# Performance work log

Hardware: AMD Instinct MI355X
Metric: run time of the kernel (lower is better)

The kernel has to match this reference:

```python
import jax, jax.numpy as jnp
import numpy as np

H, W = 16, 64
HK, WK = 7, 11
NUM_HEADS = 8
DIM = 512
HEAD_DIM = DIM // NUM_HEADS
SCALE = HEAD_DIM ** -0.5
N = H * W


def _local_mask():
    # Additive mask [N, N]: 0 inside the local window, -inf outside.
    # Equivalent to the torch loop: token (h,w) attends to (i,j) with
    # |i-h| <= HK//2 and |j-w| <= WK//2 (odd kernel, centered crop).
    h = jnp.arange(H)
    w = jnp.arange(W)
    hh, ww = jnp.meshgrid(h, w, indexing='ij')  # [H, W]
    q_h = hh.reshape(-1)  # [N]
    q_w = ww.reshape(-1)
    in_win = (jnp.abs(q_h[:, None] - q_h[None, :]) <= HK // 2) & \
             (jnp.abs(q_w[:, None] - q_w[None, :]) <= WK // 2)
    return jnp.where(in_win, 0.0, -jnp.inf).astype(jnp.float32)  # [N, N]


def setup_inputs() -> dict:
    key = jax.random.key(0)
    k1, k2, k3 = jax.random.split(key, 3)
    x = jax.random.normal(k1, (64, N, DIM), dtype=jnp.float32)
    w_qkv = jax.random.normal(k2, (DIM, 3 * DIM), dtype=jnp.float32) * 0.02
    w_proj = jax.random.normal(k3, (DIM, DIM), dtype=jnp.float32) * 0.02
    b_proj = jnp.zeros((DIM,), dtype=jnp.float32)
    return {"x": x, "w_qkv": w_qkv, "w_proj": w_proj, "b_proj": b_proj}


def reference(x, w_qkv, w_proj, b_proj):
    B = x.shape[0]
    mask = _local_mask()  # [N, N]
    qkv = (x @ w_qkv).reshape(B, N, 3, NUM_HEADS, HEAD_DIM)
    q = qkv[:, :, 0].transpose(0, 2, 1, 3) * SCALE  # [B, h, N, d]
    k = qkv[:, :, 1].transpose(0, 2, 1, 3)
    v = qkv[:, :, 2].transpose(0, 2, 1, 3)
    attn = jnp.einsum('bhnd,bhmd->bhnm', q, k) + mask  # [B, h, N, N]
    attn = jax.nn.softmax(attn, axis=-1)
    out = jnp.einsum('bhnm,bhmd->bhnd', attn, v)
    out = out.transpose(0, 2, 1, 3).reshape(B, N, DIM)
    return out @ w_proj + b_proj
```

## Files before the change

### kernel.cpp

```cpp
#include <hip/hip_runtime.h>
#include <hip/hip_bf16.h>
#include <stdint.h>

#define HGRID   16
#define WGRID   64
#define NTOK    1024
#define BATCH   64
#define NHEADS  8
#define HDIM    64
#define DMODEL  512
#define BH_TOT  512
#define QK_SCALE (0.125f * 1.44269504089f)

typedef __attribute__((ext_vector_type(8))) short short8;
typedef __attribute__((ext_vector_type(4))) float floatx4;

__device__ __forceinline__ short f2bf(float f) {
    union { float f; uint32_t u; } c{f};
    uint32_t r = (c.u + 0x7fffu + ((c.u >> 16) & 1u)) >> 16;
    return (short)r;
}

__device__ __forceinline__ void gload_lds16(const void* g, void* l) {
    auto gp = (const __attribute__((address_space(1))) void*)(uintptr_t)g;
    auto lp = (__attribute__((address_space(3))) void*)(uint32_t)(uintptr_t)l;
    __builtin_amdgcn_global_load_lds(gp, lp, 16, 0, 0);
}

__global__ __launch_bounds__(256)
void cast_x_kernel(const float* __restrict__ in, short* __restrict__ out) {
    size_t i = (size_t)blockIdx.x * 256 + threadIdx.x;
    const float4* in4 = (const float4*)in;
    float4 a = in4[i * 2];
    float4 b = in4[i * 2 + 1];
    short8 o;
    o[0] = f2bf(a.x); o[1] = f2bf(a.y); o[2] = f2bf(a.z); o[3] = f2bf(a.w);
    o[4] = f2bf(b.x); o[5] = f2bf(b.y); o[6] = f2bf(b.z); o[7] = f2bf(b.w);
    *(short8*)(out + i * 8) = o;
}

__global__ __launch_bounds__(256)
void tcast_kernel(const float* __restrict__ in, short* __restrict__ out, int R, int C) {
    __shared__ short tile[64][72];
    int r0 = blockIdx.x * 64, c0 = blockIdx.y * 64;
    int t = threadIdx.x;
#pragma unroll
    for (int i = 0; i < 16; i++) {
        int s = i * 256 + t;
        int r = s >> 6, c = s & 63;
        tile[r][c] = f2bf(in[(size_t)(r0 + r) * C + c0 + c]);
    }
    __syncthreads();
#pragma unroll
    for (int i = 0; i < 16; i++) {
        int s = i * 256 + t;
        int c = s >> 6, r = s & 63;
        out[(size_t)(c0 + c) * R + r0 + r] = tile[r][c];
    }
}

template <int MODE>
__global__ __launch_bounds__(256)
void gemm_kernel(const short* __restrict__ A, const short* __restrict__ Bm,
                 short* __restrict__ qo, short* __restrict__ ko, short* __restrict__ vo,
                 float* __restrict__ outf, const float* __restrict__ bias) {
    __shared__ short As[128 * 32];
    __shared__ short Bs[128 * 32];
    const int bn = blockIdx.x, bm = blockIdx.y;
    const int t = threadIdx.x;
    const int w = t >> 6;
    const int l = t & 63;
    const int wm = w >> 1, wn = w & 1;
    const int lq = l & 15, quad = l >> 4;

    const floatx4 zero = {0.f, 0.f, 0.f, 0.f};
    floatx4 acc[4][4];
#pragma unroll
    for (int i = 0; i < 4; i++)
#pragma unroll
        for (int j = 0; j < 4; j++) acc[i][j] = zero;

    const short* Ab = A + (size_t)bm * 128 * 512;
    const short* Bb = Bm + (size_t)bn * 128 * 512;

    for (int k0 = 0; k0 < 512; k0 += 32) {
        __syncthreads();
#pragma unroll
        for (int i = 0; i < 2; i++) {
            int s = i * 256 + t;
            int r = s >> 2, c8 = (s & 3) * 8;
            gload_lds16(Ab + (size_t)r * 512 + k0 + c8, &As[s * 8]);
            gload_lds16(Bb + (size_t)r * 512 + k0 + c8, &Bs[s * 8]);
        }
        __syncthreads();

        short8 af[4], bfr[4];
#pragma unroll
        for (int mi = 0; mi < 4; mi++)
            af[mi] = *(const short8*)&As[(wm * 64 + mi * 16 + lq) * 32 + quad * 8];
#pragma unroll
        for (int ni = 0; ni < 4; ni++)
            bfr[ni] = *(const short8*)&Bs[(wn * 64 + ni * 16 + lq) * 32 + quad * 8];
#pragma unroll
        for (int mi = 0; mi < 4; mi++)
#pragma unroll
            for (int ni = 0; ni < 4; ni++)
                acc[mi][ni] = __builtin_amdgcn_mfma_f32_16x16x32_bf16(
                    af[mi], bfr[ni], acc[mi][ni], 0, 0, 0);
    }

#pragma unroll
    for (int mi = 0; mi < 4; mi++)
#pragma unroll
        for (int ni = 0; ni < 4; ni++)
#pragma unroll
            for (int r = 0; r < 4; r++) {
                int row = bm * 128 + wm * 64 + mi * 16 + quad * 4 + r;
                int col = bn * 128 + wn * 64 + ni * 16 + lq;
                float val = acc[mi][ni][r];
                if (MODE == 0) {
                    int bidx = row >> 10, tok = row & 1023;
                    int which = col >> 9, hd = (col >> 6) & 7, dd = col & 63;
                    size_t didx = (((size_t)bidx * NHEADS + hd) * NTOK + tok) * HDIM + dd;
                    if (which == 0)       qo[didx] = f2bf(val * QK_SCALE);
                    else if (which == 1)  ko[didx] = f2bf(val);
                    else                  vo[didx] = f2bf(val);
                } else {
                    outf[(size_t)row * DMODEL + col] = val + bias[col];
                }
            }
}

__global__ __launch_bounds__(256)
void tv_kernel(const short* __restrict__ v, short* __restrict__ vT) {
    __shared__ short tile[64][72];
    int tt = blockIdx.x;
    int bh = blockIdx.y;
    int t = threadIdx.x;
    const short* src = v + ((size_t)bh * NTOK + tt * 64) * HDIM;
#pragma unroll
    for (int i = 0; i < 2; i++) {
        int s = i * 256 + t;
        int r = s >> 3, c8 = (s & 7) * 8;
        *(short8*)&tile[r][c8] = *(const short8*)(src + r * HDIM + c8);
    }
    __syncthreads();
    short* dst = vT + (size_t)bh * HDIM * NTOK + tt * 64;
#pragma unroll
    for (int i = 0; i < 2; i++) {
        int s = i * 256 + t;
        int d = s & 63, t0 = (s >> 6) * 8;
        short8 g;
#pragma unroll
        for (int j = 0; j < 8; j++) g[j] = tile[t0 + j][d];
        *(short8*)(dst + (size_t)d * NTOK + t0) = g;
    }
}

__global__ __launch_bounds__(256)
void attn_kernel(const short* __restrict__ q, const short* __restrict__ k,
                 const short* __restrict__ vT, short* __restrict__ ao) {
    const int bid = blockIdx.x;
    const int h = (bid >> 3) & 15;
    const int bh = (bid & 7) + 8 * (bid >> 7);
    const int b = bh >> 3, head = bh & 7;
    const int t = threadIdx.x;
    const int w = t >> 6;
    const int l = t & 63;
    const int lq = l & 15, quad = l >> 4;

    __shared__ short Kc[64][72];
    __shared__ short Vc[80][72];
    __shared__ short Pc[4][16][40];

    const int s_w = (w == 0) ? 0 : (w == 1) ? 8 : (w == 2) ? 24 : 32;

    const short* qbp = q + ((size_t)bh * NTOK + h * 64 + w * 16 + lq) * HDIM + quad * 8;
    short8 qa0 = *(const short8*)(qbp);
    short8 qa1 = *(const short8*)(qbp + 32);

    bool ok[2][4];
#pragma unroll
    for (int nt = 0; nt < 2; nt++)
#pragma unroll
        for (int r = 0; r < 4; r++) {
            int kw_g = s_w + nt * 16 + lq;
            int qi = w * 16 + quad * 4 + r;
            int dw = kw_g - qi;
            ok[nt][r] = (dw <= 5) && (dw >= -5);
        }

    const floatx4 zero = {0.f, 0.f, 0.f, 0.f};
    floatx4 O[5];
#pragma unroll
    for (int i = 0; i < 5; i++) O[i] = zero;

    if (t < 64) Vc[64][t] = (short)0x3F80;

    const int kh0 = (h - 3 < 0) ? 0 : h - 3;
    const int kh1 = (h + 3 > HGRID - 1) ? HGRID - 1 : h + 3;

    for (int kh = kh0; kh <= kh1; ++kh) {
        __syncthreads();
        {
            const short* kb = k + ((size_t)bh * NTOK + kh * 64) * HDIM;
            const short* vb = vT + (size_t)bh * HDIM * NTOK + kh * 64;
#pragma unroll
            for (int i = 0; i < 2; i++) {
                int s = i * 256 + t;
                int r = s >> 3, c8 = (s & 7) * 8;
                *(short8*)&Kc[r][c8] = *(const short8*)(kb + r * HDIM + c8);
                *(short8*)&Vc[r][c8] = *(const short8*)(vb + (size_t)r * NTOK + c8);
            }
        }
        __syncthreads();

        floatx4 S[2];
#pragma unroll
        for (int nt = 0; nt < 2; nt++) {
            S[nt] = zero;
            short8 b0 = *(const short8*)&Kc[s_w + nt * 16 + lq][quad * 8];
            short8 b1 = *(const short8*)&Kc[s_w + nt * 16 + lq][quad * 8 + 32];
            S[nt] = __builtin_amdgcn_mfma_f32_16x16x32_bf16(qa0, b0, S[nt], 0, 0, 0);
            S[nt] = __builtin_amdgcn_mfma_f32_16x16x32_bf16(qa1, b1, S[nt], 0, 0, 0);
        }

#pragma unroll
        for (int nt = 0; nt < 2; nt++)
#pragma unroll
            for (int r = 0; r < 4; r++) {
                float p = ok[nt][r] ? exp2f(S[nt][r]) : 0.f;
                Pc[w][quad * 4 + r][nt * 16 + lq] = f2bf(p);
            }

        short8 pa = *(const short8*)&Pc[w][lq][quad * 8];
#pragma unroll
        for (int dt = 0; dt < 5; dt++) {
            short8 vf = *(const short8*)&Vc[dt * 16 + lq][s_w + quad * 8];
            O[dt] = __builtin_amdgcn_mfma_f32_16x16x32_bf16(pa, vf, O[dt], 0, 0, 0);
        }
    }

    float inv[4];
#pragma unroll
    for (int r = 0; r < 4; r++) {
        float s = __shfl(O[4][r], l & 48);
        inv[r] = 1.0f / s;
    }

#pragma unroll
    for (int dt = 0; dt < 4; dt++)
#pragma unroll
        for (int r = 0; r < 4; r++) {
            int qi = w * 16 + quad * 4 + r;
            int d = dt * 16 + lq;
            float o = O[dt][r] * inv[r];
            ao[((size_t)b * NTOK + h * 64 + qi) * DMODEL + head * HDIM + d] = f2bf(o);
        }
}

extern "C" void kernel_launch(void* const* d_in, const int* in_sizes, int n_in,
                              void* d_out, int out_size, void* d_ws, size_t ws_size,
                              hipStream_t stream) {
    const float* x      = (const float*)d_in[0];
    const float* w_qkv  = (const float*)d_in[1];
    const float* w_proj = (const float*)d_in[2];
    const float* b_proj = (const float*)d_in[3];
    float* out = (float*)d_out;

    const size_t SZ_X    = (size_t)BATCH * NTOK * DMODEL * 2;
    const size_t SZ_HEAD = (size_t)BH_TOT * NTOK * HDIM * 2;
    char* p = (char*)d_ws;
    short* xb     = (short*)p; p += SZ_X;
    short* wqkvT  = (short*)p; p += (size_t)1536 * 512 * 2;
    short* wprojT = (short*)p; p += (size_t)512 * 512 * 2;
    short* qb     = (short*)p; p += SZ_HEAD;
    short* kb     = (short*)p; p += SZ_HEAD;
    short* vb     = (short*)p; p += SZ_HEAD;
    short* vTb    = (short*)p; p += SZ_HEAD;
    short* ao     = xb;

    cast_x_kernel<<<dim3((BATCH * NTOK * DMODEL) / (256 * 8)), dim3(256), 0, stream>>>(x, xb);
    tcast_kernel<<<dim3(512 / 64, 1536 / 64), dim3(256), 0, stream>>>(w_qkv, wqkvT, 512, 1536);
    tcast_kernel<<<dim3(512 / 64, 512 / 64), dim3(256), 0, stream>>>(w_proj, wprojT, 512, 512);
    gemm_kernel<0><<<dim3(1536 / 128, 65536 / 128), dim3(256), 0, stream>>>(
        xb, wqkvT, qb, kb, vb, nullptr, nullptr);
    tv_kernel<<<dim3(NTOK / 64, BH_TOT), dim3(256), 0, stream>>>(vb, vTb);
    attn_kernel<<<dim3(HGRID * BH_TOT), dim3(256), 0, stream>>>(qb, kb, vTb, ao);
    gemm_kernel<1><<<dim3(512 / 128, 65536 / 128), dim3(256), 0, stream>>>(
        ao, wprojT, nullptr, nullptr, nullptr, out, b_proj);
}
```

Before: 559.6 us.

## Rewrite GEMM with triple-buffered LDS pipeline and fuse V transpose into epilogue

```diff
diff --git a/kernel.cpp b/kernel.cpp
--- a/kernel.cpp
+++ b/kernel.cpp
@@ -60,18 +60,33 @@
 }
 
 template <int MODE>
-__global__ __launch_bounds__(256)
+__global__ __launch_bounds__(512, 4)
 void gemm_kernel(const short* __restrict__ A, const short* __restrict__ Bm,
-                 short* __restrict__ qo, short* __restrict__ ko, short* __restrict__ vo,
+                 short* __restrict__ qo, short* __restrict__ ko, short* __restrict__ vTo,
                  float* __restrict__ outf, const float* __restrict__ bias) {
-    __shared__ short As[128 * 32];
-    __shared__ short Bs[128 * 32];
-    const int bn = blockIdx.x, bm = blockIdx.y;
+    constexpr int NBN = (MODE == 0) ? 6 : 2;
+    constexpr int NWG = (MODE == 0) ? 3072 : 1024;
+    __shared__ char lds[73728];
+    char* ldsc = (char*)lds;
+
+    int bid = blockIdx.x;
+    bid = (bid & 7) * (NWG >> 3) + (bid >> 3);
+    const int bn = bid % NBN, bm = bid / NBN;
+
     const int t = threadIdx.x;
-    const int w = t >> 6;
-    const int l = t & 63;
-    const int wm = w >> 1, wn = w & 1;
+    const int w = t >> 6, l = t & 63;
     const int lq = l & 15, quad = l >> 4;
+    const int wm = w >> 2, wn = w & 3;
+
+    const int sw = ((quad ^ ((lq >> 1) & 3)) << 4);
+    const int a_off = (wm * 64 + lq) * 64 + sw;
+    const int b_off = 8192 + (wn * 64 + lq) * 64 + sw;
+
+    const int srow = t >> 2;
+    const int scol = ((t & 3) ^ ((t >> 3) & 3)) * 8;
+    const short* sA = A + (size_t)bm * 128 * 512 + (size_t)srow * 512 + scol;
+    const short* sB = Bm + (size_t)bn * 256 * 512 + (size_t)srow * 512 + scol;
+    const int t16 = t * 16;
 
     const floatx4 zero = {0.f, 0.f, 0.f, 0.f};
     floatx4 acc[4][4];
@@ -80,80 +95,108 @@
 #pragma unroll
         for (int j = 0; j < 4; j++) acc[i][j] = zero;
 
-    const short* Ab = A + (size_t)bm * 128 * 512;
-    const short* Bb = Bm + (size_t)bn * 128 * 512;
-
-    for (int k0 = 0; k0 < 512; k0 += 32) {
-        __syncthreads();
-#pragma unroll
-        for (int i = 0; i < 2; i++) {
-            int s = i * 256 + t;
-            int r = s >> 2, c8 = (s & 3) * 8;
-            gload_lds16(Ab + (size_t)r * 512 + k0 + c8, &As[s * 8]);
-            gload_lds16(Bb + (size_t)r * 512 + k0 + c8, &Bs[s * 8]);
-        }
-        __syncthreads();
-
+#define STAGE(T, BUFI) do {                                            \
+        char* _b = ldsc + (BUFI) * 24576;                              \
+        gload_lds16(sA + (T) * 32, _b + t16);                          \
+        gload_lds16(sB + (T) * 32, _b + 8192 + t16);                   \
+        gload_lds16(sB + 128 * 512 + (T) * 32, _b + 16384 + t16);      \
+    } while (0)
+
+    STAGE(0, 0);
+    STAGE(1, 1);
+    asm volatile("s_waitcnt vmcnt(3)" ::: "memory");
+    __builtin_amdgcn_s_barrier();
+
+#pragma unroll
+    for (int T = 0; T < 16; ++T) {
+        const int cur = T % 3;
+        if (T + 2 < 16) STAGE(T + 2, (T + 2) % 3);
+
+        const char* base = ldsc + cur * 24576;
         short8 af[4], bfr[4];
 #pragma unroll
         for (int mi = 0; mi < 4; mi++)
-            af[mi] = *(const short8*)&As[(wm * 64 + mi * 16 + lq) * 32 + quad * 8];
+            af[mi] = *(const short8*)(base + a_off + mi * 1024);
 #pragma unroll
         for (int ni = 0; ni < 4; ni++)
-            bfr[ni] = *(const short8*)&Bs[(wn * 64 + ni * 16 + lq) * 32 + quad * 8];
+            bfr[ni] = *(const short8*)(base + b_off + ni * 1024);
+        asm volatile("s_waitcnt lgkmcnt(0)" ::: "memory");
+        __builtin_amdgcn_sched_barrier(0);
+        __builtin_amdgcn_s_setprio(1);
 #pragma unroll
         for (int mi = 0; mi < 4; mi++)
 #pragma unroll
             for (int ni = 0; ni < 4; ni++)
                 acc[mi][ni] = __builtin_amdgcn_mfma_f32_16x16x32_bf16(
                     af[mi], bfr[ni], acc[mi][ni], 0, 0, 0);
-    }
-
-#pragma unroll
-    for (int mi = 0; mi < 4; mi++)
-#pragma unroll
-        for (int ni = 0; ni < 4; ni++)
-#pragma unroll
-            for (int r = 0; r < 4; r++) {
-                int row = bm * 128 + wm * 64 + mi * 16 + quad * 4 + r;
-                int col = bn * 128 + wn * 64 + ni * 16 + lq;
-                float val = acc[mi][ni][r];
-                if (MODE == 0) {
-                    int bidx = row >> 10, tok = row & 1023;
-                    int which = col >> 9, hd = (col >> 6) & 7, dd = col & 63;
-                    size_t didx = (((size_t)bidx * NHEADS + hd) * NTOK + tok) * HDIM + dd;
-                    if (which == 0)       qo[didx] = f2bf(val * QK_SCALE);
-                    else if (which == 1)  ko[didx] = f2bf(val);
-                    else                  vo[didx] = f2bf(val);
-                } else {
-                    outf[(size_t)row * DMODEL + col] = val + bias[col];
+        __builtin_amdgcn_s_setprio(0);
+        __builtin_amdgcn_sched_barrier(0);
+        if (T < 14) asm volatile("s_waitcnt vmcnt(3)" ::: "memory");
+        else        asm volatile("s_waitcnt vmcnt(0)" ::: "memory");
+        __builtin_amdgcn_s_barrier();
+    }
+#undef STAGE
+
+    if (MODE == 1) {
+#pragma unroll
+        for (int ni = 0; ni < 4; ni++) {
+            int col = bn * 256 + wn * 64 + ni * 16 + lq;
+            float bv = bias[col];
+#pragma unroll
+            for (int mi = 0; mi < 4; mi++)
+#pragma unroll
+                for (int r = 0; r < 4; r++) {
+                    int row = bm * 128 + wm * 64 + mi * 16 + quad * 4 + r;
+                    outf[(size_t)row * DMODEL + col] = acc[mi][ni][r] + bv;
+                }
+        }
+        return;
+    }
+
+    const int which = bn >> 1;
+    if (which < 2) {
+        short* dst = which ? ko : qo;
+        const float sc = which ? 1.0f : QK_SCALE;
+        const int hd = (bn & 1) * 4 + wn;
+#pragma unroll
+        for (int mi = 0; mi < 4; mi++)
+#pragma unroll
+            for (int ni = 0; ni < 4; ni++)
+#pragma unroll
+                for (int r = 0; r < 4; r++) {
+                    int row = bm * 128 + wm * 64 + mi * 16 + quad * 4 + r;
+                    int tok = row & 1023, bidx = row >> 10;
+                    dst[(((size_t)bidx * NHEADS + hd) * NTOK + tok) * HDIM + ni * 16 + lq] =
+                        f2bf(acc[mi][ni][r] * sc);
+                }
+    } else {
+        short* Tb = (short*)ldsc;
+        __syncthreads();
+#pragma unroll
+        for (int mi = 0; mi < 4; mi++)
+#pragma unroll
+            for (int ni = 0; ni < 4; ni++) {
+                int cl = wn * 64 + ni * 16 + lq;
+#pragma unroll
+                for (int rp = 0; rp < 2; rp++) {
+                    int rw = wm * 64 + mi * 16 + quad * 4 + rp * 2;
+                    uint32_t lo = (uint32_t)(uint16_t)f2bf(acc[mi][ni][rp * 2]);
+                    uint32_t hi = (uint32_t)(uint16_t)f2bf(acc[mi][ni][rp * 2 + 1]);
+                    *(uint32_t*)&Tb[cl * 140 + rw] = lo | (hi << 16);
                 }
             }
-}
-
-__global__ __launch_bounds__(256)
-void tv_kernel(const short* __restrict__ v, short* __restrict__ vT) {
-    __shared__ short tile[64][72];
-    int tt = blockIdx.x;
-    int bh = blockIdx.y;
-    int t = threadIdx.x;
-    const short* src = v + ((size_t)bh * NTOK + tt * 64) * HDIM;
-#pragma unroll
-    for (int i = 0; i < 2; i++) {
-        int s = i * 256 + t;
-        int r = s >> 3, c8 = (s & 7) * 8;
-        *(short8*)&tile[r][c8] = *(const short8*)(src + r * HDIM + c8);
-    }
-    __syncthreads();
-    short* dst = vT + (size_t)bh * HDIM * NTOK + tt * 64;
-#pragma unroll
-    for (int i = 0; i < 2; i++) {
-        int s = i * 256 + t;
-        int d = s & 63, t0 = (s >> 6) * 8;
-        short8 g;
-#pragma unroll
-        for (int j = 0; j < 8; j++) g[j] = tile[t0 + j][d];
-        *(short8*)(dst + (size_t)d * NTOK + t0) = g;
+        __syncthreads();
+        int cl = t >> 1, part = t & 1;
+        int hd = (bn & 1) * 4 + (cl >> 6), dd = cl & 63;
+        int bidx = bm >> 3, tokb = (bm & 7) * 128 + part * 64;
+        short* dst = vTo + (((size_t)bidx * NHEADS + hd) * HDIM + dd) * NTOK + tokb;
+#pragma unroll
+        for (int j = 0; j < 8; j++) {
+            uint2 x = *(const uint2*)&Tb[cl * 140 + part * 64 + j * 8];
+            uint2 y = *(const uint2*)&Tb[cl * 140 + part * 64 + j * 8 + 4];
+            uint4 o; o.x = x.x; o.y = x.y; o.z = y.x; o.w = y.y;
+            *(uint4*)(dst + j * 8) = o;
+        }
     }
 }
 
@@ -276,17 +319,13 @@
     short* wprojT = (short*)p; p += (size_t)512 * 512 * 2;
     short* qb     = (short*)p; p += SZ_HEAD;
     short* kb     = (short*)p; p += SZ_HEAD;
-    short* vb     = (short*)p; p += SZ_HEAD;
     short* vTb    = (short*)p; p += SZ_HEAD;
     short* ao     = xb;
 
     cast_x_kernel<<<dim3((BATCH * NTOK * DMODEL) / (256 * 8)), dim3(256), 0, stream>>>(x, xb);
     tcast_kernel<<<dim3(512 / 64, 1536 / 64), dim3(256), 0, stream>>>(w_qkv, wqkvT, 512, 1536);
     tcast_kernel<<<dim3(512 / 64, 512 / 64), dim3(256), 0, stream>>>(w_proj, wprojT, 512, 512);
-    gemm_kernel<0><<<dim3(1536 / 128, 65536 / 128), dim3(256), 0, stream>>>(
-        xb, wqkvT, qb, kb, vb, nullptr, nullptr);
-    tv_kernel<<<dim3(NTOK / 64, BH_TOT), dim3(256), 0, stream>>>(vb, vTb);
+    gemm_kernel<0><<<dim3(3072), dim3(512), 0, stream>>>(xb, wqkvT, qb, kb, vTb, nullptr, nullptr);
     attn_kernel<<<dim3(HGRID * BH_TOT), dim3(256), 0, stream>>>(qb, kb, vTb, ao);
-    gemm_kernel<1><<<dim3(512 / 128, 65536 / 128), dim3(256), 0, stream>>>(
-        ao, wprojT, nullptr, nullptr, nullptr, out, b_proj);
-}
+    gemm_kernel<1><<<dim3(1024), dim3(512), 0, stream>>>(ao, wprojT, nullptr, nullptr, nullptr, out, b_proj);
+}
```

Result: faster. 481.5 us (-14.0%).
